# Optimization experiments

Hardware: AMD Instinct MI355X
Metric: run time of the kernel (lower is better)

Reference implementation:

```python
import jax, jax.numpy as jnp
import numpy as np

EXPERT_NUM = 16
TOP_K = 2
BALANCE_WT = 0.01
EPS = 1e-9


def setup_inputs() -> dict:
    key = jax.random.key(0)
    ks = jax.random.split(key, 4)
    B, D, E, O = 8192, 4096, EXPERT_NUM, 512
    features = jax.random.normal(ks[0], (B, D), dtype=jnp.float32)
    W_r = jax.random.normal(ks[1], (D, E), dtype=jnp.float32) * (1.0 / np.sqrt(D))
    b_r = jnp.zeros((E,), dtype=jnp.float32)
    W_e = jax.random.normal(ks[2], (E, D, O), dtype=jnp.float32) * (1.0 / np.sqrt(D))
    b_e = jnp.zeros((E, O), dtype=jnp.float32)
    return {"features": features, "W_r": W_r, "b_r": b_r, "W_e": W_e, "b_e": b_e}


def reference(features, W_r, b_r, W_e, b_e):
    # Router: softmax over experts. [B, E]
    routing_prob = jax.nn.softmax(features @ W_r + b_r, axis=-1)
    # Top-k selection and renormalized combine weights. [B, K]
    top_values, top_indices = jax.lax.top_k(routing_prob, TOP_K)
    weights = top_values / jnp.clip(top_values.sum(axis=1, keepdims=True), EPS)
    # Dense all-expert compute (as the original does). [B, E, O]
    expert_outputs = jnp.einsum('bd,edo->beo', features, W_e) + b_e
    # Gather top-k expert outputs. [B, K, O]
    gathered = jnp.take_along_axis(expert_outputs, top_indices[:, :, None], axis=1)
    logits = jnp.sum(weights[:, :, None] * gathered, axis=1)  # [B, O]
    # Load-balance loss: KL(pi || uniform) scaled by balance_wt.
    pi = routing_prob.mean(axis=0)
    balance_loss = BALANCE_WT * (
        jnp.sum(pi * jnp.log(jnp.clip(pi, EPS)))
        + jnp.log(jnp.asarray(EXPERT_NUM, dtype=pi.dtype))
    )
    return logits, balance_loss
```

## Files before the change

kernel.cpp:

```cpp
#include <hip/hip_runtime.h>


#define B_ 8192
#define D_ 4096
#define E_ 16
#define O_ 512

typedef unsigned int uint32;
typedef unsigned short ushort_t;
typedef __bf16 bf16_t;
typedef bf16_t bf16x8 __attribute__((ext_vector_type(8)));
typedef float f32x4 __attribute__((ext_vector_type(4)));
typedef ushort_t u16x8 __attribute__((ext_vector_type(8)));

__device__ __forceinline__ uint32 bf16_rne(float x) {
  uint32 u = __float_as_uint(x);
  return (u + 0x7fffu + ((u >> 16) & 1u)) >> 16;
}
__device__ __forceinline__ float bf16_to_f32(ushort_t u) {
  return __uint_as_float(((uint32)u) << 16);
}

__device__ __forceinline__ void gload16(const void* g, void* l) {
  __builtin_amdgcn_global_load_lds(
      (const __attribute__((address_space(1))) void*)g,
      (__attribute__((address_space(3))) void*)l, 16, 0, 0);
}

__global__ __launch_bounds__(256) void wr_transpose(
    const float* __restrict__ Wr, float* __restrict__ WrT) {
  const int d = blockIdx.x * 256 + threadIdx.x;
  const f32x4* src = (const f32x4*)&Wr[(size_t)d * 16];
  f32x4 v0 = src[0], v1 = src[1], v2 = src[2], v3 = src[3];
  WrT[0 * D_ + d] = v0[0];  WrT[1 * D_ + d] = v0[1];
  WrT[2 * D_ + d] = v0[2];  WrT[3 * D_ + d] = v0[3];
  WrT[4 * D_ + d] = v1[0];  WrT[5 * D_ + d] = v1[1];
  WrT[6 * D_ + d] = v1[2];  WrT[7 * D_ + d] = v1[3];
  WrT[8 * D_ + d] = v2[0];  WrT[9 * D_ + d] = v2[1];
  WrT[10 * D_ + d] = v2[2]; WrT[11 * D_ + d] = v2[3];
  WrT[12 * D_ + d] = v3[0]; WrT[13 * D_ + d] = v3[1];
  WrT[14 * D_ + d] = v3[2]; WrT[15 * D_ + d] = v3[3];
}

__global__ __launch_bounds__(256) void we_transpose(
    const float* __restrict__ We, ushort_t* __restrict__ Wbt) {
  const int e  = blockIdx.z;
  const int d0 = blockIdx.y * 64;
  const int o0 = blockIdx.x * 64;
  __shared__ float t[64][65];
  const int tx = threadIdx.x & 15, ty = threadIdx.x >> 4;

  const float* src = We + ((size_t)e * D_ + d0) * O_ + o0;
#pragma unroll
  for (int p = 0; p < 4; ++p) {
    int dl = ty + p * 16;
    float4 v = *(const float4*)(src + (size_t)dl * O_ + tx * 4);
    t[dl][tx * 4 + 0] = v.x; t[dl][tx * 4 + 1] = v.y;
    t[dl][tx * 4 + 2] = v.z; t[dl][tx * 4 + 3] = v.w;
  }
  __syncthreads();
  ushort_t* dst = Wbt + ((size_t)e * O_ + o0) * D_ + d0;
#pragma unroll
  for (int p = 0; p < 4; ++p) {
    int ol = ty + p * 16;
    uint2 pk;
    pk.x = bf16_rne(t[tx * 4 + 0][ol]) | (bf16_rne(t[tx * 4 + 1][ol]) << 16);
    pk.y = bf16_rne(t[tx * 4 + 2][ol]) | (bf16_rne(t[tx * 4 + 3][ol]) << 16);
    *(uint2*)(dst + (size_t)ol * D_ + tx * 4) = pk;
  }
}

__global__ __launch_bounds__(256) void router_mlp(
    const float* __restrict__ feat, const float* __restrict__ WrT,
    const float* __restrict__ br, ushort_t* __restrict__ featbf,
    int* __restrict__ idxP, float2* __restrict__ wP,
    float* __restrict__ pblk) {
  __shared__ float pw[4][16];
  const int tid = threadIdx.x;
  const int lane = tid & 63, w = tid >> 6;
  const int tbase = blockIdx.x * 16 + w * 4;

  float acc[4][16] = {};

  for (int si = 0; si < 8; ++si) {
    const int d8 = si * 512 + lane * 8;
    f32x4 fa[4], fb[4];
#pragma unroll
    for (int i = 0; i < 4; ++i) {
      const float* fp = &feat[(size_t)(tbase + i) * D_ + d8];
      fa[i] = *(const f32x4*)fp;
      fb[i] = *(const f32x4*)(fp + 4);
    }
#pragma unroll
    for (int i = 0; i < 4; ++i) {
      uint4 pk;
      pk.x = bf16_rne(fa[i][0]) | (bf16_rne(fa[i][1]) << 16);
      pk.y = bf16_rne(fa[i][2]) | (bf16_rne(fa[i][3]) << 16);
      pk.z = bf16_rne(fb[i][0]) | (bf16_rne(fb[i][1]) << 16);
      pk.w = bf16_rne(fb[i][2]) | (bf16_rne(fb[i][3]) << 16);
      *(uint4*)&featbf[(size_t)(tbase + i) * D_ + d8] = pk;
    }
#pragma unroll
    for (int e = 0; e < 16; ++e) {
      const float* wp = &WrT[(size_t)e * D_ + d8];
      f32x4 wa = *(const f32x4*)wp;
      f32x4 wb = *(const f32x4*)(wp + 4);
#pragma unroll
      for (int i = 0; i < 4; ++i) {
        float a = acc[i][e];
        a = fmaf(fa[i][0], wa[0], a);
        a = fmaf(fa[i][1], wa[1], a);
        a = fmaf(fa[i][2], wa[2], a);
        a = fmaf(fa[i][3], wa[3], a);
        a = fmaf(fb[i][0], wb[0], a);
        a = fmaf(fb[i][1], wb[1], a);
        a = fmaf(fb[i][2], wb[2], a);
        a = fmaf(fb[i][3], wb[3], a);
        acc[i][e] = a;
      }
    }
  }

  float psum[16];
#pragma unroll
  for (int e = 0; e < 16; ++e) psum[e] = 0.f;

#pragma unroll
  for (int i = 0; i < 4; ++i) {
    float l[16];
#pragma unroll
    for (int e = 0; e < 16; ++e) {
      float v = acc[i][e];
#pragma unroll
      for (int m = 32; m >= 1; m >>= 1) v += __shfl_xor(v, m, 64);
      l[e] = v + br[e];
    }
    float mx = l[0];
#pragma unroll
    for (int e = 1; e < 16; ++e) mx = fmaxf(mx, l[e]);
    float p[16];
    float s = 0.f;
#pragma unroll
    for (int e = 0; e < 16; ++e) { p[e] = expf(l[e] - mx); s += p[e]; }
    float inv = 1.f / s;
#pragma unroll
    for (int e = 0; e < 16; ++e) { p[e] *= inv; psum[e] += p[e]; }
    int i0 = 0; float v0 = p[0];
#pragma unroll
    for (int e = 1; e < 16; ++e) if (p[e] > v0) { v0 = p[e]; i0 = e; }
    int i1 = (i0 == 0) ? 1 : 0; float v1 = p[i1];
#pragma unroll
    for (int e = 0; e < 16; ++e)
      if (e != i0 && p[e] > v1) { v1 = p[e]; i1 = e; }
    float denom = fmaxf(v0 + v1, 1e-9f);
    if (lane == 0) {
      int t = tbase + i;
      idxP[t] = i0 | (i1 << 8);
      wP[t] = make_float2(v0 / denom, v1 / denom);
    }
  }
  if (lane == 0) {
#pragma unroll
    for (int e = 0; e < 16; ++e) pw[w][e] = psum[e];
  }
  __syncthreads();
  if (tid < 16)
    pblk[blockIdx.x * 16 + tid] =
        (pw[0][tid] + pw[1][tid]) + (pw[2][tid] + pw[3][tid]);
}

__global__ __launch_bounds__(256) void bucket(
    const int* __restrict__ idxP, const float2* __restrict__ wP,
    int* __restrict__ tokL, float* __restrict__ wgtL, int* __restrict__ cntA,
    int* __restrict__ posA, int* __restrict__ posB) {
  const int e = blockIdx.x;
  const int tid = threadIdx.x, lane = tid & 63, w = tid >> 6;
  __shared__ int wsum[4];
  __shared__ int basev;
  if (tid == 0) basev = 0;
  __syncthreads();

  for (int c = 0; c < B_; c += 256) {
    const int t = c + tid;
    const int pk = idxP[t];
    const float2 wv = wP[t];
    const bool m0 = (pk & 255) == e;
    const bool m1 = (pk >> 8) == e;
    const bool m = m0 || m1;
    const float wt = m0 ? wv.x : wv.y;
    unsigned long long bal = __ballot(m);
    int rank = __popcll(bal & ((1ull << lane) - 1ull));
    if (lane == 0) wsum[w] = __popcll(bal);
    __syncthreads();
    int wbase = basev;
    for (int q = 0; q < w; ++q) wbase += wsum[q];
    if (m) {
      int pos = wbase + rank;
      tokL[e * B_ + pos] = t;
      wgtL[e * B_ + pos] = wt;
      if (m0) posA[t] = pos; else posB[t] = pos;
    }
    __syncthreads();
    if (tid == 0) basev += (wsum[0] + wsum[1]) + (wsum[2] + wsum[3]);
  }
  __syncthreads();
  if (tid == 0) cntA[e] = basev;
}

#define VM3 asm volatile("s_waitcnt vmcnt(3)" ::: "memory")
#define VM0 asm volatile("s_waitcnt vmcnt(0)" ::: "memory")

__global__ __launch_bounds__(512, 4) void moe_gemm(
    const ushort_t* __restrict__ featbf, const ushort_t* __restrict__ Wbt,
    const float* __restrict__ be, const int* __restrict__ tokL,
    const float* __restrict__ wgtL, const int* __restrict__ cntA,
    ushort_t* __restrict__ g0, ushort_t* __restrict__ g1,
    float* __restrict__ out, int dense) {
  const int orig = blockIdx.x;
  const int work = (orig & 7) * 512 + (orig >> 3);
  const int z = work >> 7;
  const int e = z >> 1, khalf = z & 1;
  const int cnt = cntA[e];
  const int row0 = ((work >> 1) & 63) * 128;
  if (row0 >= cnt) return;
  const int o0 = (work & 1) * 256;

  const int tid = threadIdx.x;
  const int lane = tid & 63, w = tid >> 6;
  const int wm = w >> 2, wn = w & 3;

  __shared__ __align__(16) ushort_t As[3][128 * 32];
  __shared__ __align__(16) ushort_t Bs[3][256 * 32];

  const int kg = (lane & 3) ^ ((lane >> 3) & 3);
  const size_t kbase = (size_t)khalf * 2048 + kg * 8;
  const int arow = row0 + w * 16 + (lane >> 2);
  const int atok = (arow < cnt) ? tokL[e * B_ + arow] : 0;
  const ushort_t* aS = featbf + (size_t)atok * D_ + kbase;
  const ushort_t* bS[2];
#pragma unroll
  for (int j = 0; j < 2; ++j) {
    int r = (2 * w + j) * 16 + (lane >> 2);
    bS[j] = Wbt + ((size_t)e * O_ + o0 + r) * D_ + kbase;
  }

  f32x4 acc[4][4] = {};
  const int lr = lane & 15;
  const int lg = lane >> 4;
  const int ps = (lg ^ ((lr >> 1) & 3)) * 8;

#define STAGE(buf, t)                                                \
  {                                                                  \
    gload16(aS + (t) * 32, &As[buf][(w * 16) * 32]);                 \
    gload16(bS[0] + (t) * 32, &Bs[buf][(2 * w) * 512]);              \
    gload16(bS[1] + (t) * 32, &Bs[buf][(2 * w + 1) * 512]);          \
  }

#define COMPUTE(buf)                                                 \
  {                                                                  \
    bf16x8 af[4], bf[4];                                             \
    _Pragma("unroll") for (int m = 0; m < 4; ++m)                    \
        af[m] = *(const bf16x8*)&As[buf][(wm * 64 + m * 16 + lr) * 32 + ps]; \
    _Pragma("unroll") for (int n = 0; n < 4; ++n)                    \
        bf[n] = *(const bf16x8*)&Bs[buf][(wn * 64 + n * 16 + lr) * 32 + ps]; \
    __builtin_amdgcn_s_setprio(1);                                   \
    _Pragma("unroll") for (int m = 0; m < 4; ++m)                    \
        _Pragma("unroll") for (int n = 0; n < 4; ++n)                \
            acc[m][n] = __builtin_amdgcn_mfma_f32_16x16x32_bf16(     \
                af[m], bf[n], acc[m][n], 0, 0, 0);                   \
    __builtin_amdgcn_s_setprio(0);                                   \
  }

  STAGE(0, 0);
  STAGE(1, 1);
  for (int tt = 0; tt < 20; ++tt) {
    const int t = tt * 3;
    VM3; __builtin_amdgcn_s_barrier(); STAGE(2, t + 2); COMPUTE(0);
    VM3; __builtin_amdgcn_s_barrier(); STAGE(0, t + 3); COMPUTE(1);
    VM3; __builtin_amdgcn_s_barrier(); STAGE(1, t + 4); COMPUTE(2);
  }
  VM3; __builtin_amdgcn_s_barrier(); STAGE(2, 62); COMPUTE(0);
  VM3; __builtin_amdgcn_s_barrier(); STAGE(0, 63); COMPUTE(1);
  VM3; __builtin_amdgcn_s_barrier(); COMPUTE(2);
  VM0; __builtin_amdgcn_s_barrier(); COMPUTE(0);

  if (dense) {
    int base = 0;
#pragma unroll
    for (int j = 0; j < 16; ++j) base += (j < e) ? cntA[j] : 0;
    ushort_t* G = khalf ? g1 : g0;
#pragma unroll
    for (int m = 0; m < 4; ++m) {
#pragma unroll
      for (int i = 0; i < 4; ++i) {
        int gr = row0 + wm * 64 + m * 16 + (lane >> 4) * 4 + i;
        if (gr < cnt) {
#pragma unroll
          for (int n = 0; n < 4; ++n) {
            int o = o0 + wn * 64 + n * 16 + (lane & 15);
            G[(size_t)(base + gr) * O_ + o] = (ushort_t)bf16_rne(acc[m][n][i]);
          }
        }
      }
    }
  } else {
#pragma unroll
    for (int m = 0; m < 4; ++m) {
#pragma unroll
      for (int i = 0; i < 4; ++i) {
        int gr = row0 + wm * 64 + m * 16 + (lane >> 4) * 4 + i;
        if (gr < cnt) {
          int tk = tokL[e * B_ + gr];
          float wt = wgtL[e * B_ + gr];
#pragma unroll
          for (int n = 0; n < 4; ++n) {
            int o = o0 + wn * 64 + n * 16 + (lane & 15);
            float v = acc[m][n][i] + (khalf ? 0.f : be[e * O_ + o]);
            atomicAdd(&out[(size_t)tk * O_ + o], wt * v);
          }
        }
      }
    }
  }
#undef STAGE
#undef COMPUTE
}

__global__ __launch_bounds__(256) void combine(
    const ushort_t* __restrict__ g0, const ushort_t* __restrict__ g1,
    const int* __restrict__ idxP, const float2* __restrict__ wP,
    const int* __restrict__ posA, const int* __restrict__ posB,
    const int* __restrict__ cntA, const float* __restrict__ be,
    const float* __restrict__ pblk, float* __restrict__ out) {
  const int tid = threadIdx.x;
  const int t = blockIdx.x * 4 + (tid >> 6);
  const int o = (tid & 63) * 8;
  const int pk = idxP[t];
  const int e0 = pk & 255, e1 = pk >> 8;
  const float2 wv = wP[t];
  int s = 0, off0 = 0, off1 = 0;
#pragma unroll
  for (int j = 0; j < 16; ++j) {
    if (j == e0) off0 = s;
    if (j == e1) off1 = s;
    s += cntA[j];
  }
  const size_t s0 = (size_t)(off0 + posA[t]) * O_ + o;
  const size_t s1 = (size_t)(off1 + posB[t]) * O_ + o;
  u16x8 a0 = *(const u16x8*)&g0[s0];
  u16x8 a1 = *(const u16x8*)&g1[s0];
  u16x8 b0 = *(const u16x8*)&g0[s1];
  u16x8 b1 = *(const u16x8*)&g1[s1];
  const float* be0 = &be[e0 * O_ + o];
  const float* be1 = &be[e1 * O_ + o];
  float r[8];
#pragma unroll
  for (int j = 0; j < 8; ++j) {
    float a = bf16_to_f32(a0[j]) + bf16_to_f32(a1[j]) + be0[j];
    float b = bf16_to_f32(b0[j]) + bf16_to_f32(b1[j]) + be1[j];
    r[j] = wv.x * a + wv.y * b;
  }
  *(f32x4*)&out[(size_t)t * O_ + o] =
      f32x4{r[0], r[1], r[2], r[3]};
  *(f32x4*)&out[(size_t)t * O_ + o + 4] =
      f32x4{r[4], r[5], r[6], r[7]};

  if (blockIdx.x == 0) {
    __shared__ float red[64];
    if (tid < 64) {
      const int e = tid & 15, g = tid >> 4;
      float acc = 0.f;
      for (int b = g; b < 512; b += 4) acc += pblk[b * 16 + e];
      red[tid] = acc;
    }
    __syncthreads();
    if (tid < 16) {
      float tot = (red[tid] + red[16 + tid]) + (red[32 + tid] + red[48 + tid]);
      float pi = tot * (1.f / (float)B_);
      red[tid] = pi * logf(fmaxf(pi, 1e-9f));
    }
    __syncthreads();
    if (tid == 0) {
      float loss = 0.f;
#pragma unroll
      for (int e2 = 0; e2 < 16; ++e2) loss += red[e2];
      out[(size_t)B_ * O_] = 0.01f * (loss + logf(16.f));
    }
  }
}

__global__ __launch_bounds__(64) void finalize(const float* __restrict__ pblk,
                                               float* __restrict__ out) {
  __shared__ float red[64];
  const int tid = threadIdx.x;
  const int e = tid & 15, g = tid >> 4;
  float s = 0.f;
  for (int b = g; b < 512; b += 4) s += pblk[b * 16 + e];
  red[tid] = s;
  __syncthreads();
  if (tid < 16) {
    float tot = (red[tid] + red[16 + tid]) + (red[32 + tid] + red[48 + tid]);
    float pi = tot * (1.f / (float)B_);
    red[tid] = pi * logf(fmaxf(pi, 1e-9f));
  }
  __syncthreads();
  if (tid == 0) {
    float loss = 0.f;
#pragma unroll
    for (int e2 = 0; e2 < 16; ++e2) loss += red[e2];
    out[(size_t)B_ * O_] = 0.01f * (loss + logf(16.f));
  }
}

extern "C" void kernel_launch(void* const* d_in, const int* in_sizes, int n_in,
                              void* d_out, int out_size, void* d_ws,
                              size_t ws_size, hipStream_t stream) {
  const float* feat = (const float*)d_in[0];
  const float* Wr = (const float*)d_in[1];
  const float* br = (const float*)d_in[2];
  const float* We = (const float*)d_in[3];
  const float* be = (const float*)d_in[4];
  float* out = (float*)d_out;

  char* ws = (char*)d_ws;
  const size_t SZG     = (size_t)(2 * B_) * O_ * 2;
  const size_t OFF_FEAT = 67108864;
  const size_t OFF_G0   = OFF_FEAT + 67108864;
  const size_t OFF_G1   = OFF_G0 + SZG;
  const size_t OFF_TOK  = OFF_G1 + SZG;
  const size_t OFF_WGT  = OFF_TOK + 524288;
  const size_t OFF_CNT  = OFF_WGT + 524288;
  const size_t OFF_IDX  = OFF_CNT + 256;
  const size_t OFF_WP   = OFF_IDX + 32768;
  const size_t OFF_PB   = OFF_WP + 65536;
  const size_t OFF_PA   = OFF_PB + 32768;
  const size_t OFF_PBo  = OFF_PA + 32768;
  const size_t OFF_WRT  = OFF_PBo + 32768;
  const size_t NEED     = OFF_WRT + 262144;
  ushort_t* Wbt = (ushort_t*)ws;
  ushort_t* featbf = (ushort_t*)(ws + OFF_FEAT);
  ushort_t* g0 = (ushort_t*)(ws + OFF_G0);
  ushort_t* g1 = (ushort_t*)(ws + OFF_G1);
  int* tokL = (int*)(ws + OFF_TOK);
  float* wgtL = (float*)(ws + OFF_WGT);
  int* cntA = (int*)(ws + OFF_CNT);
  int* idxP = (int*)(ws + OFF_IDX);
  float2* wP = (float2*)(ws + OFF_WP);
  float* pblk = (float*)(ws + OFF_PB);
  int* posA = (int*)(ws + OFF_PA);
  int* posB = (int*)(ws + OFF_PBo);
  float* WrT = (float*)(ws + OFF_WRT);
  const int dense = ws_size >= NEED ? 1 : 0;

  if (!dense)
    hipMemsetAsync(out, 0, (size_t)(B_ * O_ + 1) * sizeof(float), stream);

  wr_transpose<<<D_ / 256, 256, 0, stream>>>(Wr, WrT);
  router_mlp<<<B_ / 16, 256, 0, stream>>>(feat, WrT, br, featbf, idxP, wP,
                                          pblk);
  bucket<<<E_, 256, 0, stream>>>(idxP, wP, tokL, wgtL, cntA, posA, posB);
  we_transpose<<<dim3(O_ / 64, D_ / 64, E_), 256, 0, stream>>>(We, Wbt);
  moe_gemm<<<4096, 512, 0, stream>>>(featbf, Wbt, be, tokL, wgtL, cntA, g0,
                                     g1, out, dense);
  if (dense)
    combine<<<B_ / 4, 256, 0, stream>>>(g0, g1, idxP, wP, posA, posB, cntA,
                                        be, pblk, out);
  else
    finalize<<<1, 64, 0, stream>>>(pblk, out);
}
```

Baseline: 305.0 us.

## Merge router and expert-weight transpose into one prep kernel; reorder compute before staging

The router/softmax/top-k kernel and the expert-weight fp32-to-bf16 transpose now run as one launch, with block ranges split by blockIdx, so the two independent memory-bound jobs can overlap on the GPU. Each transpose block now handles four tiles, reusing one shared buffer. Separately, the GEMM main loop issues the MFMA compute before the next stage's global-to-LDS loads, changing how loads and compute overlap. The fused kernel's shared memory size follows the larger transpose tile, which may lower occupancy for the router blocks.

New measurement: 265.7 us. -12.9%, faster.

```diff
diff --git a/kernel.cpp b/kernel.cpp
--- a/kernel.cpp
+++ b/kernel.cpp
@@ -42,131 +42,141 @@
   WrT[14 * D_ + d] = v3[2]; WrT[15 * D_ + d] = v3[3];
 }
 
-__global__ __launch_bounds__(256) void we_transpose(
-    const float* __restrict__ We, ushort_t* __restrict__ Wbt) {
-  const int e  = blockIdx.z;
-  const int d0 = blockIdx.y * 64;
-  const int o0 = blockIdx.x * 64;
-  __shared__ float t[64][65];
-  const int tx = threadIdx.x & 15, ty = threadIdx.x >> 4;
-
-  const float* src = We + ((size_t)e * D_ + d0) * O_ + o0;
-#pragma unroll
-  for (int p = 0; p < 4; ++p) {
-    int dl = ty + p * 16;
-    float4 v = *(const float4*)(src + (size_t)dl * O_ + tx * 4);
-    t[dl][tx * 4 + 0] = v.x; t[dl][tx * 4 + 1] = v.y;
-    t[dl][tx * 4 + 2] = v.z; t[dl][tx * 4 + 3] = v.w;
-  }
-  __syncthreads();
-  ushort_t* dst = Wbt + ((size_t)e * O_ + o0) * D_ + d0;
-#pragma unroll
-  for (int p = 0; p < 4; ++p) {
-    int ol = ty + p * 16;
-    uint2 pk;
-    pk.x = bf16_rne(t[tx * 4 + 0][ol]) | (bf16_rne(t[tx * 4 + 1][ol]) << 16);
-    pk.y = bf16_rne(t[tx * 4 + 2][ol]) | (bf16_rne(t[tx * 4 + 3][ol]) << 16);
-    *(uint2*)(dst + (size_t)ol * D_ + tx * 4) = pk;
-  }
-}
-
-__global__ __launch_bounds__(256) void router_mlp(
+__global__ __launch_bounds__(256) void prep(
     const float* __restrict__ feat, const float* __restrict__ WrT,
-    const float* __restrict__ br, ushort_t* __restrict__ featbf,
+    const float* __restrict__ br, const float* __restrict__ We,
+    ushort_t* __restrict__ featbf, ushort_t* __restrict__ Wbt,
     int* __restrict__ idxP, float2* __restrict__ wP,
     float* __restrict__ pblk) {
-  __shared__ float pw[4][16];
+  __shared__ __align__(16) float shmem[64 * 65];
   const int tid = threadIdx.x;
-  const int lane = tid & 63, w = tid >> 6;
-  const int tbase = blockIdx.x * 16 + w * 4;
-
-  float acc[4][16] = {};
-
-  for (int si = 0; si < 8; ++si) {
-    const int d8 = si * 512 + lane * 8;
-    f32x4 fa[4], fb[4];
+
+  if (blockIdx.x < 512) {
+    const int lane = tid & 63, w = tid >> 6;
+    const int tbase = blockIdx.x * 16 + w * 4;
+
+    float acc[4][16] = {};
+
+    for (int si = 0; si < 8; ++si) {
+      const int d8 = si * 512 + lane * 8;
+      f32x4 fa[4], fb[4];
+#pragma unroll
+      for (int i = 0; i < 4; ++i) {
+        const float* fp = &feat[(size_t)(tbase + i) * D_ + d8];
+        fa[i] = *(const f32x4*)fp;
+        fb[i] = *(const f32x4*)(fp + 4);
+      }
+#pragma unroll
+      for (int i = 0; i < 4; ++i) {
+        uint4 pk;
+        pk.x = bf16_rne(fa[i][0]) | (bf16_rne(fa[i][1]) << 16);
+        pk.y = bf16_rne(fa[i][2]) | (bf16_rne(fa[i][3]) << 16);
+        pk.z = bf16_rne(fb[i][0]) | (bf16_rne(fb[i][1]) << 16);
+        pk.w = bf16_rne(fb[i][2]) | (bf16_rne(fb[i][3]) << 16);
+        *(uint4*)&featbf[(size_t)(tbase + i) * D_ + d8] = pk;
+      }
+#pragma unroll
+      for (int e = 0; e < 16; ++e) {
+        const float* wp = &WrT[(size_t)e * D_ + d8];
+        f32x4 wa = *(const f32x4*)wp;
+        f32x4 wb = *(const f32x4*)(wp + 4);
+#pragma unroll
+        for (int i = 0; i < 4; ++i) {
+          float a = acc[i][e];
+          a = fmaf(fa[i][0], wa[0], a);
+          a = fmaf(fa[i][1], wa[1], a);
+          a = fmaf(fa[i][2], wa[2], a);
+          a = fmaf(fa[i][3], wa[3], a);
+          a = fmaf(fb[i][0], wb[0], a);
+          a = fmaf(fb[i][1], wb[1], a);
+          a = fmaf(fb[i][2], wb[2], a);
+          a = fmaf(fb[i][3], wb[3], a);
+          acc[i][e] = a;
+        }
+      }
+    }
+
+    float psum[16];
+#pragma unroll
+    for (int e = 0; e < 16; ++e) psum[e] = 0.f;
+
 #pragma unroll
     for (int i = 0; i < 4; ++i) {
-      const float* fp = &feat[(size_t)(tbase + i) * D_ + d8];
-      fa[i] = *(const f32x4*)fp;
-      fb[i] = *(const f32x4*)(fp + 4);
-    }
-#pragma unroll
-    for (int i = 0; i < 4; ++i) {
-      uint4 pk;
-      pk.x = bf16_rne(fa[i][0]) | (bf16_rne(fa[i][1]) << 16);
-      pk.y = bf16_rne(fa[i][2]) | (bf16_rne(fa[i][3]) << 16);
-      pk.z = bf16_rne(fb[i][0]) | (bf16_rne(fb[i][1]) << 16);
-      pk.w = bf16_rne(fb[i][2]) | (bf16_rne(fb[i][3]) << 16);
-      *(uint4*)&featbf[(size_t)(tbase + i) * D_ + d8] = pk;
-    }
-#pragma unroll
-    for (int e = 0; e < 16; ++e) {
-      const float* wp = &WrT[(size_t)e * D_ + d8];
-      f32x4 wa = *(const f32x4*)wp;
-      f32x4 wb = *(const f32x4*)(wp + 4);
-#pragma unroll
-      for (int i = 0; i < 4; ++i) {
-        float a = acc[i][e];
-        a = fmaf(fa[i][0], wa[0], a);
-        a = fmaf(fa[i][1], wa[1], a);
-        a = fmaf(fa[i][2], wa[2], a);
-        a = fmaf(fa[i][3], wa[3], a);
-        a = fmaf(fb[i][0], wb[0], a);
-        a = fmaf(fb[i][1], wb[1], a);
-        a = fmaf(fb[i][2], wb[2], a);
-        a = fmaf(fb[i][3], wb[3], a);
-        acc[i][e] = a;
-      }
-    }
-  }
-
-  float psum[16];
-#pragma unroll
-  for (int e = 0; e < 16; ++e) psum[e] = 0.f;
-
-#pragma unroll
-  for (int i = 0; i < 4; ++i) {
-    float l[16];
-#pragma unroll
-    for (int e = 0; e < 16; ++e) {
-      float v = acc[i][e];
-#pragma unroll
-      for (int m = 32; m >= 1; m >>= 1) v += __shfl_xor(v, m, 64);
-      l[e] = v + br[e];
-    }
-    float mx = l[0];
-#pragma unroll
-    for (int e = 1; e < 16; ++e) mx = fmaxf(mx, l[e]);
-    float p[16];
-    float s = 0.f;
-#pragma unroll
-    for (int e = 0; e < 16; ++e) { p[e] = expf(l[e] - mx); s += p[e]; }
-    float inv = 1.f / s;
-#pragma unroll
-    for (int e = 0; e < 16; ++e) { p[e] *= inv; psum[e] += p[e]; }
-    int i0 = 0; float v0 = p[0];
-#pragma unroll
-    for (int e = 1; e < 16; ++e) if (p[e] > v0) { v0 = p[e]; i0 = e; }
-    int i1 = (i0 == 0) ? 1 : 0; float v1 = p[i1];
-#pragma unroll
-    for (int e = 0; e < 16; ++e)
-      if (e != i0 && p[e] > v1) { v1 = p[e]; i1 = e; }
-    float denom = fmaxf(v0 + v1, 1e-9f);
+      float l[16];
+#pragma unroll
+      for (int e = 0; e < 16; ++e) {
+        float v = acc[i][e];
+#pragma unroll
+        for (int m = 32; m >= 1; m >>= 1) v += __shfl_xor(v, m, 64);
+        l[e] = v + br[e];
+      }
+      float mx = l[0];
+#pragma unroll
+      for (int e = 1; e < 16; ++e) mx = fmaxf(mx, l[e]);
+      float p[16];
+      float s = 0.f;
+#pragma unroll
+      for (int e = 0; e < 16; ++e) { p[e] = expf(l[e] - mx); s += p[e]; }
+      float inv = 1.f / s;
+#pragma unroll
+      for (int e = 0; e < 16; ++e) { p[e] *= inv; psum[e] += p[e]; }
+      int i0 = 0; float v0 = p[0];
+#pragma unroll
+      for (int e = 1; e < 16; ++e) if (p[e] > v0) { v0 = p[e]; i0 = e; }
+      int i1 = (i0 == 0) ? 1 : 0; float v1 = p[i1];
+#pragma unroll
+      for (int e = 0; e < 16; ++e)
+        if (e != i0 && p[e] > v1) { v1 = p[e]; i1 = e; }
+      float denom = fmaxf(v0 + v1, 1e-9f);
+      if (lane == 0) {
+        int t = tbase + i;
+        idxP[t] = i0 | (i1 << 8);
+        wP[t] = make_float2(v0 / denom, v1 / denom);
+      }
+    }
     if (lane == 0) {
-      int t = tbase + i;
-      idxP[t] = i0 | (i1 << 8);
-      wP[t] = make_float2(v0 / denom, v1 / denom);
-    }
-  }
-  if (lane == 0) {
-#pragma unroll
-    for (int e = 0; e < 16; ++e) pw[w][e] = psum[e];
-  }
-  __syncthreads();
-  if (tid < 16)
-    pblk[blockIdx.x * 16 + tid] =
-        (pw[0][tid] + pw[1][tid]) + (pw[2][tid] + pw[3][tid]);
+#pragma unroll
+      for (int e = 0; e < 16; ++e) shmem[w * 16 + e] = psum[e];
+    }
+    __syncthreads();
+    if (tid < 16)
+      pblk[blockIdx.x * 16 + tid] =
+          (shmem[tid] + shmem[16 + tid]) + (shmem[32 + tid] + shmem[48 + tid]);
+  } else {
+    const int tx = tid & 15, ty = tid >> 4;
+    const int wid = blockIdx.x - 512;
+#pragma unroll
+    for (int q = 0; q < 4; ++q) {
+      const int tix = wid * 4 + q;
+      const int e = tix >> 9;
+      const int rem = tix & 511;
+      const int d0 = (rem >> 3) << 6;
+      const int o0 = (rem & 7) << 6;
+      const float* src = We + ((size_t)e * D_ + d0) * O_ + o0;
+      if (q) __syncthreads();
+#pragma unroll
+      for (int p = 0; p < 4; ++p) {
+        int dl = ty + p * 16;
+        float4 v = *(const float4*)(src + (size_t)dl * O_ + tx * 4);
+        shmem[dl * 65 + tx * 4 + 0] = v.x;
+        shmem[dl * 65 + tx * 4 + 1] = v.y;
+        shmem[dl * 65 + tx * 4 + 2] = v.z;
+        shmem[dl * 65 + tx * 4 + 3] = v.w;
+      }
+      __syncthreads();
+      ushort_t* dst = Wbt + ((size_t)e * O_ + o0) * D_ + d0;
+#pragma unroll
+      for (int p = 0; p < 4; ++p) {
+        int ol = ty + p * 16;
+        uint2 pk;
+        pk.x = bf16_rne(shmem[(tx * 4 + 0) * 65 + ol]) |
+               (bf16_rne(shmem[(tx * 4 + 1) * 65 + ol]) << 16);
+        pk.y = bf16_rne(shmem[(tx * 4 + 2) * 65 + ol]) |
+               (bf16_rne(shmem[(tx * 4 + 3) * 65 + ol]) << 16);
+        *(uint2*)(dst + (size_t)ol * D_ + tx * 4) = pk;
+      }
+    }
+  }
 }
 
 __global__ __launch_bounds__(256) void bucket(
@@ -275,12 +285,12 @@
   STAGE(1, 1);
   for (int tt = 0; tt < 20; ++tt) {
     const int t = tt * 3;
-    VM3; __builtin_amdgcn_s_barrier(); STAGE(2, t + 2); COMPUTE(0);
-    VM3; __builtin_amdgcn_s_barrier(); STAGE(0, t + 3); COMPUTE(1);
-    VM3; __builtin_amdgcn_s_barrier(); STAGE(1, t + 4); COMPUTE(2);
-  }
-  VM3; __builtin_amdgcn_s_barrier(); STAGE(2, 62); COMPUTE(0);
-  VM3; __builtin_amdgcn_s_barrier(); STAGE(0, 63); COMPUTE(1);
+    VM3; __builtin_amdgcn_s_barrier(); COMPUTE(0); STAGE(2, t + 2);
+    VM3; __builtin_amdgcn_s_barrier(); COMPUTE(1); STAGE(0, t + 3);
+    VM3; __builtin_amdgcn_s_barrier(); COMPUTE(2); STAGE(1, t + 4);
+  }
+  VM3; __builtin_amdgcn_s_barrier(); COMPUTE(0); STAGE(2, 62);
+  VM3; __builtin_amdgcn_s_barrier(); COMPUTE(1); STAGE(0, 63);
   VM3; __builtin_amdgcn_s_barrier(); COMPUTE(2);
   VM0; __builtin_amdgcn_s_barrier(); COMPUTE(0);
 
@@ -360,10 +370,8 @@
     float b = bf16_to_f32(b0[j]) + bf16_to_f32(b1[j]) + be1[j];
     r[j] = wv.x * a + wv.y * b;
   }
-  *(f32x4*)&out[(size_t)t * O_ + o] =
-      f32x4{r[0], r[1], r[2], r[3]};
-  *(f32x4*)&out[(size_t)t * O_ + o + 4] =
-      f32x4{r[4], r[5], r[6], r[7]};
+  *(f32x4*)&out[(size_t)t * O_ + o] = f32x4{r[0], r[1], r[2], r[3]};
+  *(f32x4*)&out[(size_t)t * O_ + o + 4] = f32x4{r[4], r[5], r[6], r[7]};
 
   if (blockIdx.x == 0) {
     __shared__ float red[64];
@@ -456,10 +464,9 @@
     hipMemsetAsync(out, 0, (size_t)(B_ * O_ + 1) * sizeof(float), stream);
 
   wr_transpose<<<D_ / 256, 256, 0, stream>>>(Wr, WrT);
-  router_mlp<<<B_ / 16, 256, 0, stream>>>(feat, WrT, br, featbf, idxP, wP,
-                                          pblk);
+  prep<<<512 + 2048, 256, 0, stream>>>(feat, WrT, br, We, featbf, Wbt, idxP,
+                                       wP, pblk);
   bucket<<<E_, 256, 0, stream>>>(idxP, wP, tokL, wgtL, cntA, posA, posB);
-  we_transpose<<<dim3(O_ / 64, D_ / 64, E_), 256, 0, stream>>>(We, Wbt);
   moe_gemm<<<4096, 512, 0, stream>>>(featbf, Wbt, be, tokL, wgtL, cntA, g0,
                                      g1, out, dense);
   if (dense)
```
